# Optimization experiments

Hardware: AMD Instinct MI355X
Metric: run time of the kernel (lower is better)

The kernel has to match this reference:

```python
import jax, jax.numpy as jnp
import numpy as np

N_HEAD = 16
N_EMBD = 1024
CHUNK = 64
ROPE_BASE = 10000.0


def setup_inputs() -> dict:
    key = jax.random.key(0)
    k1, k2, k3 = jax.random.split(key, 3)
    B, T, C = 4, 4096, N_EMBD
    x = jax.random.normal(k1, (B, T, C), dtype=jnp.float32)
    # torch nn.Linear weights: (out_features, in_features), init-scale ~ 1/sqrt(C)
    w_attn = jax.random.normal(k2, (3 * C, C), dtype=jnp.float32) / np.sqrt(C)
    w_proj = jax.random.normal(k3, (C, C), dtype=jnp.float32) / np.sqrt(C)
    return {"x": x, "w_attn": w_attn, "w_proj": w_proj}


def _rope_tables(head_dim, chunk_size, dtype):
    # positions restart every chunk (Rotary with chunk_size)
    inv_freq = 1.0 / (ROPE_BASE ** (jnp.arange(0, head_dim, 2, dtype=jnp.float32) / head_dim))
    t = jnp.arange(chunk_size, dtype=jnp.float32)
    freqs = jnp.outer(t, inv_freq)  # (chunk, d/2)
    return jnp.cos(freqs).astype(dtype), jnp.sin(freqs).astype(dtype)


def _apply_rope(x, cos, sin):
    # x: (B, nc, chunk, H, d); cos/sin: (chunk, d/2)
    d = x.shape[-1] // 2
    x1, x2 = x[..., :d], x[..., d:]
    c = cos[None, None, :, None, :]
    s = sin[None, None, :, None, :]
    return jnp.concatenate([x1 * c + x2 * s, -x1 * s + x2 * c], axis=-1)


def reference(x, w_attn, w_proj):
    B, T, C = x.shape
    H, cs = N_HEAD, CHUNK
    d = C // H
    nc = T // cs
    qkv = jnp.einsum('btc,fc->btf', x, w_attn)
    q, k, v = jnp.split(qkv, 3, axis=2)
    # reshape to (B, n_chunks, chunk, H, d) — chunks are independent
    q = q.reshape(B, nc, cs, H, d)
    k = k.reshape(B, nc, cs, H, d)
    v = v.reshape(B, nc, cs, H, d)
    cos, sin = _rope_tables(d, cs, x.dtype)
    q = _apply_rope(q, cos, sin)
    k = _apply_rope(k, cos, sin)
    scale = 1.0 / np.sqrt(d)
    scores = jnp.einsum('bnqhd,bnkhd->bnhqk', q, k) * scale  # (B,nc,H,cs,cs)
    p = jax.nn.softmax(scores, axis=-1)
    y = jnp.einsum('bnhqk,bnkhd->bnqhd', p, v)
    y = y.reshape(B, T, C)
    return jnp.einsum('btc,oc->bto', y, w_proj)
```

## Files before the change

### kernel.cpp

```cpp
#include <hip/hip_runtime.h>
#include <math.h>

typedef __attribute__((ext_vector_type(8))) short short8;
typedef __attribute__((ext_vector_type(4))) short s16x4;
typedef __attribute__((ext_vector_type(4))) float floatx4;

__device__ __forceinline__ float bits2f(short u) {
  unsigned int x = ((unsigned int)(unsigned short)u) << 16;
  return __builtin_bit_cast(float, x);
}
__device__ __forceinline__ short f2bits(float f) {
  unsigned int x = __builtin_bit_cast(unsigned int, f);
  x += 0x7FFFu + ((x >> 16) & 1u);
  return (short)(x >> 16);
}

__device__ __forceinline__ void gload_lds16(const short* g, short* l) {
  __builtin_amdgcn_global_load_lds((const __attribute__((address_space(1))) void*)g,
                                   (__attribute__((address_space(3))) void*)l, 16, 0, 0);
}

__global__ __launch_bounds__(256) void cvt_bf16(const float* __restrict__ in,
                                                short* __restrict__ out, long n8) {
  long i = (long)blockIdx.x * 256 + threadIdx.x;
  const long stride = (long)gridDim.x * 256;
  for (; i < n8; i += stride) {
    const floatx4* p = (const floatx4*)(in + i * 8);
    floatx4 v0 = p[0], v1 = p[1];
    short8 o;
#pragma unroll
    for (int e = 0; e < 4; e++) { o[e] = f2bits(v0[e]); o[e + 4] = f2bits(v1[e]); }
    *(short8*)(out + i * 8) = o;
  }
}

__global__ __launch_bounds__(256) void rope_table(float* __restrict__ tab) {
  int i = blockIdx.x * 256 + threadIdx.x;
  if (i >= 64 * 32) return;
  int t = i >> 5, j = i & 31;
  float inv = exp2f(-(float)j * 0.41524101186092030f);
  float ang = (float)t * inv;
  tab[i * 2]     = cosf(ang);
  tab[i * 2 + 1] = sinf(ang);
}

template <bool COUT_F32>
__global__ __launch_bounds__(512, 2) void gemm256(const short* __restrict__ A,
                                                  const short* __restrict__ B,
                                                  void* __restrict__ C,
                                                  int M, int N, int K) {
  (void)M;
  __shared__ __attribute__((aligned(16))) short lds[65536];

  const int t    = threadIdx.x;
  const int lane = t & 63;
  const int wave = t >> 6;
  const int wm   = wave >> 2;
  const int wn   = wave & 3;
  const int frow = lane & 15;
  const int quad = lane >> 4;

  const int nwg = gridDim.x;
  const int cpx = nwg >> 3;
  const int bid = blockIdx.x;
  const int swz = (bid & 7) * cpx + (bid >> 3);
  const int nbx = N >> 8;
  const int bx  = swz % nbx;
  const int by  = swz / nbx;
  const long m0 = (long)by * 256;
  const long n0 = (long)bx * 256;

  const int NT = K >> 5;

  const int  srow  = t >> 2;
  const int  scol  = ((t & 3) ^ ((srow >> 1) & 3)) * 8;
  const long aoff0 = (m0 + srow) * (long)K + scol;
  const long aoff1 = aoff0 + 128L * K;
  const long boff0 = (n0 + srow) * (long)K + scol;
  const long boff1 = boff0 + 128L * K;
  const int  t8    = t * 8;

  const int sw8 = (quad ^ ((frow >> 1) & 3)) * 8;

  floatx4 acc[8][4];
#pragma unroll
  for (int i = 0; i < 8; i++)
#pragma unroll
    for (int j = 0; j < 4; j++) acc[i][j] = (floatx4){0.f, 0.f, 0.f, 0.f};

  for (int p = 0; p < 3; ++p) {
    short* la = lds + p * 16384;
    const long kk = (long)p * 32;
    gload_lds16(A + aoff0 + kk, la + t8);
    gload_lds16(A + aoff1 + kk, la + t8 + 4096);
    gload_lds16(B + boff0 + kk, la + 8192 + t8);
    gload_lds16(B + boff1 + kk, la + 8192 + t8 + 4096);
  }

#define GSTEP(KT, VMSTR, DO_STAGE)                                                     \
  {                                                                                    \
    const int kt_ = (KT);                                                              \
    asm volatile("s_barrier" ::: "memory");     \
    if (DO_STAGE) {                                                                    \
      short* sa = lds + ((kt_ + 3) & 3) * 16384;                                       \
      const long kk = (long)(kt_ + 3) * 32;                                            \
      gload_lds16(A + aoff0 + kk, sa + t8);                                            \
      gload_lds16(A + aoff1 + kk, sa + t8 + 4096);                                     \
    }                                                                                  \
    asm volatile("s_waitcnt " VMSTR ::: "memory");   \
    asm volatile("s_barrier" ::: "memory");               \
    {                                                                                  \
      const short* la = lds + (kt_ & 3) * 16384;                                       \
      const short* lb = la + 8192;                                                     \
      short8 af[8], bf[4];                                                             \
      _Pragma("unroll")                                                                \
      for (int ni = 0; ni < 4; ni++)                                                   \
        bf[ni] = *(const short8*)&lb[(wn * 64 + ni * 16 + frow) * 32 + sw8];           \
      _Pragma("unroll")                                                                \
      for (int mi = 0; mi < 8; mi++)                                                   \
        af[mi] = *(const short8*)&la[(wm * 128 + mi * 16 + frow) * 32 + sw8];          \
      __builtin_amdgcn_s_setprio(1);                                                   \
      _Pragma("unroll")                                                                \
      for (int mi = 0; mi < 4; mi++)                                                   \
        _Pragma("unroll")                                                              \
        for (int ni = 0; ni < 4; ni++)                                                 \
          acc[mi][ni] =                                                                \
              __builtin_amdgcn_mfma_f32_16x16x32_bf16(af[mi], bf[ni], acc[mi][ni], 0, 0, 0); \
      __builtin_amdgcn_s_setprio(0);                                                   \
      if (DO_STAGE) {                                                                  \
        short* sb = lds + ((kt_ + 3) & 3) * 16384;                                     \
        const long kk = (long)(kt_ + 3) * 32;                                          \
        gload_lds16(B + boff0 + kk, sb + 8192 + t8);                                   \
        gload_lds16(B + boff1 + kk, sb + 8192 + t8 + 4096);                            \
      }                                                                                \
      __builtin_amdgcn_s_setprio(1);                                                   \
      _Pragma("unroll")                                                                \
      for (int mi = 4; mi < 8; mi++)                                                   \
        _Pragma("unroll")                                                              \
        for (int ni = 0; ni < 4; ni++)                                                 \
          acc[mi][ni] =                                                                \
              __builtin_amdgcn_mfma_f32_16x16x32_bf16(af[mi], bf[ni], acc[mi][ni], 0, 0, 0); \
      __builtin_amdgcn_s_setprio(0);                                                   \
    }                                                                                  \
  }

  for (int kt = 0; kt <= NT - 4; ++kt) GSTEP(kt, "vmcnt(10)", true);
  GSTEP(NT - 3, "vmcnt(8)", false);
  GSTEP(NT - 2, "vmcnt(4)", false);
  GSTEP(NT - 1, "vmcnt(0)", false);
#undef GSTEP

  const long mrow0 = m0 + wm * 128;
  const long ncol0 = n0 + wn * 64;
#pragma unroll
  for (int mi = 0; mi < 8; mi++)
#pragma unroll
    for (int ni = 0; ni < 4; ni++) {
      long row0 = mrow0 + mi * 16 + quad * 4;
      long col  = ncol0 + ni * 16 + frow;
#pragma unroll
      for (int r = 0; r < 4; r++) {
        if constexpr (COUT_F32)
          ((float*)C)[(row0 + r) * (long)N + col] = acc[mi][ni][r];
        else
          ((short*)C)[(row0 + r) * (long)N + col] = f2bits(acc[mi][ni][r]);
      }
    }
}

__global__ __launch_bounds__(64, 1) void attn_mfma(const short* __restrict__ qkv,
                                                   short* __restrict__ y,
                                                   const float* __restrict__ cstab) {
  const int lane = threadIdx.x;
  const int frow = lane & 15;
  const int quad = lane >> 4;
  const int h = blockIdx.x, chunk = blockIdx.y, b = blockIdx.z;
  const long rowbase = (long)b * 4096 + (long)chunk * 64;

  __shared__ __attribute__((aligned(16))) short vt[64][68];
  __shared__ __attribute__((aligned(16))) short ps[64][68];

  const short* qb = qkv + rowbase * 3072 + h * 64;

  short8 qf[4][2], kf[4][2];
#pragma unroll
  for (int i = 0; i < 4; i++) {
    const short* rq = qb + (long)(16 * i + frow) * 3072 + quad * 8;
    qf[i][0] = *(const short8*)(rq);
    qf[i][1] = *(const short8*)(rq + 32);
    kf[i][0] = *(const short8*)(rq + 1024);
    kf[i][1] = *(const short8*)(rq + 1056);
    const floatx4* tp = (const floatx4*)(cstab + ((16 * i + frow) * 32 + quad * 8) * 2);
    floatx4 tv0 = tp[0], tv1 = tp[1], tv2 = tp[2], tv3 = tp[3];
#define CS_(k) ((k) < 4 ? tv0[(k) & 3] : (k) < 8 ? tv1[(k) & 3] : (k) < 12 ? tv2[(k) & 3] : tv3[(k) & 3])
#pragma unroll
    for (int e = 0; e < 8; e++) {
      float c = CS_(2 * e), s = CS_(2 * e + 1);
      float a0 = bits2f(qf[i][0][e]), a1 = bits2f(qf[i][1][e]);
      qf[i][0][e] = f2bits(a0 * c + a1 * s);
      qf[i][1][e] = f2bits(a1 * c - a0 * s);
      float b0 = bits2f(kf[i][0][e]), b1 = bits2f(kf[i][1][e]);
      kf[i][0][e] = f2bits(b0 * c + b1 * s);
      kf[i][1][e] = f2bits(b1 * c - b0 * s);
    }
#undef CS_
  }

  const short* vb = qb + 2048 + (long)lane * 3072;
#pragma unroll
  for (int w = 0; w < 8; w++) {
    short8 v8 = *(const short8*)(vb + w * 8);
#pragma unroll
    for (int e = 0; e < 8; e++) vt[w * 8 + e][lane] = v8[e];
  }
  __syncthreads();

  floatx4 sc[4][4];
#pragma unroll
  for (int mi = 0; mi < 4; mi++)
#pragma unroll
    for (int ni = 0; ni < 4; ni++) {
      sc[mi][ni] = (floatx4){0.f, 0.f, 0.f, 0.f};
      sc[mi][ni] = __builtin_amdgcn_mfma_f32_16x16x32_bf16(qf[mi][0], kf[ni][0], sc[mi][ni], 0, 0, 0);
      sc[mi][ni] = __builtin_amdgcn_mfma_f32_16x16x32_bf16(qf[mi][1], kf[ni][1], sc[mi][ni], 0, 0, 0);
    }

  float is_[4][4];
#pragma unroll
  for (int mi = 0; mi < 4; mi++)
#pragma unroll
    for (int r = 0; r < 4; r++) {
      float mx = fmaxf(fmaxf(sc[mi][0][r], sc[mi][1][r]), fmaxf(sc[mi][2][r], sc[mi][3][r]));
      mx = fmaxf(mx, __shfl_xor(mx, 1));
      mx = fmaxf(mx, __shfl_xor(mx, 2));
      mx = fmaxf(mx, __shfl_xor(mx, 4));
      mx = fmaxf(mx, __shfl_xor(mx, 8));
      float sm = 0.f;
#pragma unroll
      for (int ni = 0; ni < 4; ni++) {
        float e_ = __expf((sc[mi][ni][r] - mx) * 0.125f);
        sc[mi][ni][r] = e_;
        sm += e_;
      }
      sm += __shfl_xor(sm, 1);
      sm += __shfl_xor(sm, 2);
      sm += __shfl_xor(sm, 4);
      sm += __shfl_xor(sm, 8);
      is_[mi][r] = 1.0f / sm;
    }

#pragma unroll
  for (int mi = 0; mi < 4; mi++)
#pragma unroll
    for (int ni = 0; ni < 4; ni++)
#pragma unroll
      for (int r = 0; r < 4; r++)
        ps[mi * 16 + quad * 4 + r][ni * 16 + frow] = f2bits(sc[mi][ni][r] * is_[mi][r]);
  __syncthreads();

  short8 pf[4][2], vf[4][2];
#pragma unroll
  for (int i = 0; i < 4; i++)
#pragma unroll
    for (int ks = 0; ks < 2; ks++) {
      const short* pp = &ps[frow + 16 * i][quad * 8 + 32 * ks];
      s16x4 p0 = *(const s16x4*)pp, p1 = *(const s16x4*)(pp + 4);
      const short* vp = &vt[frow + 16 * i][quad * 8 + 32 * ks];
      s16x4 v0 = *(const s16x4*)vp, v1 = *(const s16x4*)(vp + 4);
#pragma unroll
      for (int e = 0; e < 4; e++) {
        pf[i][ks][e] = p0[e]; pf[i][ks][e + 4] = p1[e];
        vf[i][ks][e] = v0[e]; vf[i][ks][e + 4] = v1[e];
      }
    }

  floatx4 oc[4][4];
#pragma unroll
  for (int mi = 0; mi < 4; mi++)
#pragma unroll
    for (int ni = 0; ni < 4; ni++) {
      oc[mi][ni] = (floatx4){0.f, 0.f, 0.f, 0.f};
      oc[mi][ni] = __builtin_amdgcn_mfma_f32_16x16x32_bf16(pf[mi][0], vf[ni][0], oc[mi][ni], 0, 0, 0);
      oc[mi][ni] = __builtin_amdgcn_mfma_f32_16x16x32_bf16(pf[mi][1], vf[ni][1], oc[mi][ni], 0, 0, 0);
    }

#pragma unroll
  for (int mi = 0; mi < 4; mi++)
#pragma unroll
    for (int ni = 0; ni < 4; ni++)
#pragma unroll
      for (int r = 0; r < 4; r++)
        y[(rowbase + mi * 16 + quad * 4 + r) * 1024 + h * 64 + ni * 16 + frow] =
            f2bits(oc[mi][ni][r]);
}

extern "C" void kernel_launch(void* const* d_in, const int* in_sizes, int n_in,
                              void* d_out, int out_size, void* d_ws, size_t ws_size,
                              hipStream_t stream) {
  (void)in_sizes; (void)n_in; (void)out_size; (void)ws_size;
  const float* x      = (const float*)d_in[0];
  const float* w_attn = (const float*)d_in[1];
  const float* w_proj = (const float*)d_in[2];
  float* out = (float*)d_out;

  short* qkv = (short*)d_ws;
  short* yb  = qkv + (size_t)16384 * 3072;
  short* wab = yb;
  short* wpb = qkv;
  short* xb  = (short*)d_out;
  float* tab = (float*)((char*)d_out + (size_t)32 * 1024 * 1024);

  cvt_bf16<<<dim3(2048), 256, 0, stream>>>(x,      xb,  (long)16384 * 1024 / 8);
  cvt_bf16<<<dim3(1024), 256, 0, stream>>>(w_attn, wab, (long)3072 * 1024 / 8);
  rope_table<<<dim3(8), 256, 0, stream>>>(tab);
  gemm256<false><<<dim3(768), 512, 0, stream>>>(xb, wab, qkv, 16384, 3072, 1024);
  attn_mfma<<<dim3(16, 64, 4), 64, 0, stream>>>(qkv, yb, tab);
  cvt_bf16<<<dim3(512), 256, 0, stream>>>(w_proj, wpb, (long)1024 * 1024 / 8);
  gemm256<true><<<dim3(256), 512, 0, stream>>>(yb, wpb, out, 16384, 1024, 1024);
}
```

Measured before the change: 300.8 us.

## Split attention per chunk-head into four query-stripe blocks

The attention kernel now launches four single-wave blocks per (head, chunk), each handling a 16-row query stripe instead of all 64 rows. This quadruples the grid and cuts per-block register use, aiming for more occupancy and latency hiding. In exchange, each block redundantly loads and ropes the full K and V tiles, so K/V global traffic and the rope work on K grow about fourfold.

New measurement: 370.7 us. 23.2% more time.

```diff
diff --git a/kernel.cpp b/kernel.cpp
--- a/kernel.cpp
+++ b/kernel.cpp
@@ -168,43 +168,55 @@
     }
 }
 
-__global__ __launch_bounds__(64, 1) void attn_mfma(const short* __restrict__ qkv,
-                                                   short* __restrict__ y,
-                                                   const float* __restrict__ cstab) {
+__global__ __launch_bounds__(64, 1) void attn_stripe(const short* __restrict__ qkv,
+                                                     short* __restrict__ y,
+                                                     const float* __restrict__ cstab) {
   const int lane = threadIdx.x;
   const int frow = lane & 15;
   const int quad = lane >> 4;
-  const int h = blockIdx.x, chunk = blockIdx.y, b = blockIdx.z;
+  const int h = blockIdx.x >> 2, qs = blockIdx.x & 3;
+  const int chunk = blockIdx.y, b = blockIdx.z;
   const long rowbase = (long)b * 4096 + (long)chunk * 64;
 
   __shared__ __attribute__((aligned(16))) short vt[64][68];
-  __shared__ __attribute__((aligned(16))) short ps[64][68];
+  __shared__ __attribute__((aligned(16))) short ps[16][68];
 
   const short* qb = qkv + rowbase * 3072 + h * 64;
 
-  short8 qf[4][2], kf[4][2];
+#define CS_(k) ((k) < 4 ? tv0[(k) & 3] : (k) < 8 ? tv1[(k) & 3] : (k) < 12 ? tv2[(k) & 3] : tv3[(k) & 3])
+  short8 qf[2];
+  {
+    const short* rq = qb + (long)(16 * qs + frow) * 3072 + quad * 8;
+    qf[0] = *(const short8*)(rq);
+    qf[1] = *(const short8*)(rq + 32);
+    const floatx4* tp = (const floatx4*)(cstab + ((16 * qs + frow) * 32 + quad * 8) * 2);
+    floatx4 tv0 = tp[0], tv1 = tp[1], tv2 = tp[2], tv3 = tp[3];
+#pragma unroll
+    for (int e = 0; e < 8; e++) {
+      float c = CS_(2 * e), s = CS_(2 * e + 1);
+      float a0 = bits2f(qf[0][e]), a1 = bits2f(qf[1][e]);
+      qf[0][e] = f2bits(a0 * c + a1 * s);
+      qf[1][e] = f2bits(a1 * c - a0 * s);
+    }
+  }
+
+  short8 kf[4][2];
 #pragma unroll
   for (int i = 0; i < 4; i++) {
-    const short* rq = qb + (long)(16 * i + frow) * 3072 + quad * 8;
-    qf[i][0] = *(const short8*)(rq);
-    qf[i][1] = *(const short8*)(rq + 32);
-    kf[i][0] = *(const short8*)(rq + 1024);
-    kf[i][1] = *(const short8*)(rq + 1056);
+    const short* rk = qb + (long)(16 * i + frow) * 3072 + quad * 8;
+    kf[i][0] = *(const short8*)(rk + 1024);
+    kf[i][1] = *(const short8*)(rk + 1056);
     const floatx4* tp = (const floatx4*)(cstab + ((16 * i + frow) * 32 + quad * 8) * 2);
     floatx4 tv0 = tp[0], tv1 = tp[1], tv2 = tp[2], tv3 = tp[3];
-#define CS_(k) ((k) < 4 ? tv0[(k) & 3] : (k) < 8 ? tv1[(k) & 3] : (k) < 12 ? tv2[(k) & 3] : tv3[(k) & 3])
 #pragma unroll
     for (int e = 0; e < 8; e++) {
       float c = CS_(2 * e), s = CS_(2 * e + 1);
-      float a0 = bits2f(qf[i][0][e]), a1 = bits2f(qf[i][1][e]);
-      qf[i][0][e] = f2bits(a0 * c + a1 * s);
-      qf[i][1][e] = f2bits(a1 * c - a0 * s);
       float b0 = bits2f(kf[i][0][e]), b1 = bits2f(kf[i][1][e]);
       kf[i][0][e] = f2bits(b0 * c + b1 * s);
       kf[i][1][e] = f2bits(b1 * c - b0 * s);
     }
+  }
 #undef CS_
-  }
 
   const short* vb = qb + 2048 + (long)lane * 3072;
 #pragma unroll
@@ -215,83 +227,75 @@
   }
   __syncthreads();
 
-  floatx4 sc[4][4];
-#pragma unroll
-  for (int mi = 0; mi < 4; mi++)
+  floatx4 sc[4];
+#pragma unroll
+  for (int ni = 0; ni < 4; ni++) {
+    sc[ni] = (floatx4){0.f, 0.f, 0.f, 0.f};
+    sc[ni] = __builtin_amdgcn_mfma_f32_16x16x32_bf16(qf[0], kf[ni][0], sc[ni], 0, 0, 0);
+    sc[ni] = __builtin_amdgcn_mfma_f32_16x16x32_bf16(qf[1], kf[ni][1], sc[ni], 0, 0, 0);
+  }
+
+  float is_[4];
+#pragma unroll
+  for (int r = 0; r < 4; r++) {
+    float mx = fmaxf(fmaxf(sc[0][r], sc[1][r]), fmaxf(sc[2][r], sc[3][r]));
+    mx = fmaxf(mx, __shfl_xor(mx, 1));
+    mx = fmaxf(mx, __shfl_xor(mx, 2));
+    mx = fmaxf(mx, __shfl_xor(mx, 4));
+    mx = fmaxf(mx, __shfl_xor(mx, 8));
+    float sm = 0.f;
 #pragma unroll
     for (int ni = 0; ni < 4; ni++) {
-      sc[mi][ni] = (floatx4){0.f, 0.f, 0.f, 0.f};
-      sc[mi][ni] = __builtin_amdgcn_mfma_f32_16x16x32_bf16(qf[mi][0], kf[ni][0], sc[mi][ni], 0, 0, 0);
-      sc[mi][ni] = __builtin_amdgcn_mfma_f32_16x16x32_bf16(qf[mi][1], kf[ni][1], sc[mi][ni], 0, 0, 0);
-    }
-
-  float is_[4][4];
-#pragma unroll
-  for (int mi = 0; mi < 4; mi++)
-#pragma unroll
-    for (int r = 0; r < 4; r++) {
-      float mx = fmaxf(fmaxf(sc[mi][0][r], sc[mi][1][r]), fmaxf(sc[mi][2][r], sc[mi][3][r]));
-      mx = fmaxf(mx, __shfl_xor(mx, 1));
-      mx = fmaxf(mx, __shfl_xor(mx, 2));
-      mx = fmaxf(mx, __shfl_xor(mx, 4));
-      mx = fmaxf(mx, __shfl_xor(mx, 8));
-      float sm = 0.f;
-#pragma unroll
-      for (int ni = 0; ni < 4; ni++) {
-        float e_ = __expf((sc[mi][ni][r] - mx) * 0.125f);
-        sc[mi][ni][r] = e_;
-        sm += e_;
-      }
-      sm += __shfl_xor(sm, 1);
-      sm += __shfl_xor(sm, 2);
-      sm += __shfl_xor(sm, 4);
-      sm += __shfl_xor(sm, 8);
-      is_[mi][r] = 1.0f / sm;
-    }
-
-#pragma unroll
-  for (int mi = 0; mi < 4; mi++)
-#pragma unroll
-    for (int ni = 0; ni < 4; ni++)
-#pragma unroll
-      for (int r = 0; r < 4; r++)
-        ps[mi * 16 + quad * 4 + r][ni * 16 + frow] = f2bits(sc[mi][ni][r] * is_[mi][r]);
+      float e_ = __expf((sc[ni][r] - mx) * 0.125f);
+      sc[ni][r] = e_;
+      sm += e_;
+    }
+    sm += __shfl_xor(sm, 1);
+    sm += __shfl_xor(sm, 2);
+    sm += __shfl_xor(sm, 4);
+    sm += __shfl_xor(sm, 8);
+    is_[r] = 1.0f / sm;
+  }
+
+#pragma unroll
+  for (int ni = 0; ni < 4; ni++)
+#pragma unroll
+    for (int r = 0; r < 4; r++)
+      ps[quad * 4 + r][ni * 16 + frow] = f2bits(sc[ni][r] * is_[r]);
   __syncthreads();
 
-  short8 pf[4][2], vf[4][2];
-#pragma unroll
-  for (int i = 0; i < 4; i++)
+  short8 pf[2], vf[4][2];
+#pragma unroll
+  for (int ks = 0; ks < 2; ks++) {
+    const short* pp = &ps[frow][quad * 8 + 32 * ks];
+    s16x4 p0 = *(const s16x4*)pp, p1 = *(const s16x4*)(pp + 4);
+#pragma unroll
+    for (int e = 0; e < 4; e++) { pf[ks][e] = p0[e]; pf[ks][e + 4] = p1[e]; }
+  }
+#pragma unroll
+  for (int ni = 0; ni < 4; ni++)
 #pragma unroll
     for (int ks = 0; ks < 2; ks++) {
-      const short* pp = &ps[frow + 16 * i][quad * 8 + 32 * ks];
-      s16x4 p0 = *(const s16x4*)pp, p1 = *(const s16x4*)(pp + 4);
-      const short* vp = &vt[frow + 16 * i][quad * 8 + 32 * ks];
+      const short* vp = &vt[ni * 16 + frow][quad * 8 + 32 * ks];
       s16x4 v0 = *(const s16x4*)vp, v1 = *(const s16x4*)(vp + 4);
 #pragma unroll
-      for (int e = 0; e < 4; e++) {
-        pf[i][ks][e] = p0[e]; pf[i][ks][e + 4] = p1[e];
-        vf[i][ks][e] = v0[e]; vf[i][ks][e + 4] = v1[e];
-      }
-    }
-
-  floatx4 oc[4][4];
-#pragma unroll
-  for (int mi = 0; mi < 4; mi++)
-#pragma unroll
-    for (int ni = 0; ni < 4; ni++) {
-      oc[mi][ni] = (floatx4){0.f, 0.f, 0.f, 0.f};
-      oc[mi][ni] = __builtin_amdgcn_mfma_f32_16x16x32_bf16(pf[mi][0], vf[ni][0], oc[mi][ni], 0, 0, 0);
-      oc[mi][ni] = __builtin_amdgcn_mfma_f32_16x16x32_bf16(pf[mi][1], vf[ni][1], oc[mi][ni], 0, 0, 0);
-    }
-
-#pragma unroll
-  for (int mi = 0; mi < 4; mi++)
-#pragma unroll
-    for (int ni = 0; ni < 4; ni++)
-#pragma unroll
-      for (int r = 0; r < 4; r++)
-        y[(rowbase + mi * 16 + quad * 4 + r) * 1024 + h * 64 + ni * 16 + frow] =
-            f2bits(oc[mi][ni][r]);
+      for (int e = 0; e < 4; e++) { vf[ni][ks][e] = v0[e]; vf[ni][ks][e + 4] = v1[e]; }
+    }
+
+  floatx4 oc[4];
+#pragma unroll
+  for (int ni = 0; ni < 4; ni++) {
+    oc[ni] = (floatx4){0.f, 0.f, 0.f, 0.f};
+    oc[ni] = __builtin_amdgcn_mfma_f32_16x16x32_bf16(pf[0], vf[ni][0], oc[ni], 0, 0, 0);
+    oc[ni] = __builtin_amdgcn_mfma_f32_16x16x32_bf16(pf[1], vf[ni][1], oc[ni], 0, 0, 0);
+  }
+
+#pragma unroll
+  for (int ni = 0; ni < 4; ni++)
+#pragma unroll
+    for (int r = 0; r < 4; r++)
+      y[(rowbase + 16 * qs + quad * 4 + r) * 1024 + h * 64 + ni * 16 + frow] =
+          f2bits(oc[ni][r]);
 }
 
 extern "C" void kernel_launch(void* const* d_in, const int* in_sizes, int n_in,
@@ -314,7 +318,7 @@
   cvt_bf16<<<dim3(1024), 256, 0, stream>>>(w_attn, wab, (long)3072 * 1024 / 8);
   rope_table<<<dim3(8), 256, 0, stream>>>(tab);
   gemm256<false><<<dim3(768), 512, 0, stream>>>(xb, wab, qkv, 16384, 3072, 1024);
-  attn_mfma<<<dim3(16, 64, 4), 64, 0, stream>>>(qkv, yb, tab);
+  attn_stripe<<<dim3(64, 64, 4), 64, 0, stream>>>(qkv, yb, tab);
   cvt_bf16<<<dim3(512), 256, 0, stream>>>(w_proj, wpb, (long)1024 * 1024 / 8);
   gemm256<true><<<dim3(256), 512, 0, stream>>>(yb, wpb, out, 16384, 1024, 1024);
 }
```
